# Kernel optimization log

Measured on AMD Instinct MI355X. Metric: run time of the kernel, lower is better.

Reference implementation:

```python
import jax, jax.numpy as jnp
import numpy as np
from jax import lax

BETA = 0.8
THRESHOLD = 1.0
SURROGATE_ALPHA = 4.0  # slope of sigmoid surrogate gradient
EPS = 1e-12            # matches torch F.normalize eps

@jax.custom_vjp
def surrogate_spike(m):
    # forward: hard threshold at THRESHOLD
    return (m >= THRESHOLD).astype(m.dtype)

def _spike_fwd(m):
    return surrogate_spike(m), m

def _spike_bwd(m, g):
    # sigmoid-derivative surrogate gradient around threshold
    s = jax.nn.sigmoid(SURROGATE_ALPHA * (m - THRESHOLD))
    return (g * SURROGATE_ALPHA * s * (1.0 - s),)

surrogate_spike.defvjp(_spike_fwd, _spike_bwd)

def _l2_normalize(x):
    n = jnp.sqrt(jnp.sum(x * x, axis=-1, keepdims=True))
    return x / jnp.maximum(n, EPS)

def setup_inputs() -> dict:
    key = jax.random.key(0)
    k1, k2, k3 = jax.random.split(key, 3)
    B, T, D, F = 4, 2048, 1024, 4096
    mlp_input = jax.random.normal(k1, (B, T, D), dtype=jnp.float32)
    mlp_activation = jax.random.normal(k2, (B, T, F), dtype=jnp.float32)
    W_proj = jax.random.normal(k3, (F, D), dtype=jnp.float32) * (1.0 / np.sqrt(D))
    theta = jnp.ones((F,), dtype=jnp.float32) * THRESHOLD
    return {"mlp_input": mlp_input, "mlp_activation": mlp_activation,
            "W_proj": W_proj, "theta": theta}

def reference(mlp_input, mlp_activation, W_proj, theta):
    B, T, D = mlp_input.shape
    Fdim = W_proj.shape[0]
    # gate_input: (B, T, d_ff) = mlp_input @ W^T
    gate_input = jnp.einsum('btd,fd->btf', mlp_input, W_proj)

    def step(mem, g_t):
        mem = BETA * mem + g_t               # leaky integrate
        spk = surrogate_spike(mem)           # fire
        mem = mem - theta * spk              # soft reset
        return mem, spk

    mem0 = jnp.zeros((B, Fdim), dtype=gate_input.dtype)
    # scan over time: (T, B, d_ff)
    _, spikes = lax.scan(step, mem0, jnp.swapaxes(gate_input, 0, 1))
    lif_gate = jnp.swapaxes(spikes, 0, 1)    # (B, T, d_ff)

    norm_mlp = _l2_normalize(mlp_activation)
    norm_lif = _l2_normalize(lif_gate)
    # cosine similarity of two (already) unit vectors == dot product
    cos = jnp.sum(norm_mlp * norm_lif, axis=-1)
    return 1.0 - jnp.mean(cos)
```

## Files before the change

### kernel.cpp

```cpp
#include <hip/hip_runtime.h>
#include <hip/hip_bf16.h>

typedef unsigned short u16;
typedef unsigned char  u8;
typedef unsigned int   u32;
typedef unsigned long long u64;
typedef __attribute__((ext_vector_type(4)))  int i32x4;
typedef __attribute__((ext_vector_type(16))) int i32x16;

#define T_LEN    2048
#define NB       4
#define K_DIM    1024
#define F_DIM    4096
#define M_FULL   (NB * T_LEN)
#define BETA_C   0.8f
#define THRESH_C 1.0f
#define S8DEC    (6.0f / 127.0f)
#define A_ENC    (127.0f / 6.0f)
#define W_ENC    (127.0f / 0.1875f)
#define C_QUANT  (0.1875f / 127.0f)

__device__ static inline u32 q8pack(float4 v, float s) {
    int q0 = (int)rintf(fminf(fmaxf(v.x * s, -127.f), 127.f));
    int q1 = (int)rintf(fminf(fmaxf(v.y * s, -127.f), 127.f));
    int q2 = (int)rintf(fminf(fmaxf(v.z * s, -127.f), 127.f));
    int q3 = (int)rintf(fminf(fmaxf(v.w * s, -127.f), 127.f));
    return (u32)(q0 & 255) | ((u32)(q1 & 255) << 8) | ((u32)(q2 & 255) << 16) |
           ((u32)(q3 & 255) << 24);
}

__global__ __launch_bounds__(256) void cvt8_kernel(const float* __restrict__ a,
                                                   const float* __restrict__ w,
                                                   u8* __restrict__ oa,
                                                   u8* __restrict__ ow,
                                                   int n4a, int n4tot) {
    int stride = gridDim.x * blockDim.x;
    for (int i = blockIdx.x * blockDim.x + threadIdx.x; i < n4tot; i += stride) {
        bool isA = (i < n4a);
        int j = isA ? i : (i - n4a);
        float4 v = isA ? ((const float4*)a)[j] : ((const float4*)w)[j];
        u32 p = q8pack(v, isA ? A_ENC : W_ENC);
        if (isA) ((u32*)oa)[j] = p; else ((u32*)ow)[j] = p;
    }
}

__device__ static inline void gload_lds16(const void* g, void* l) {
    __builtin_amdgcn_global_load_lds(
        (const __attribute__((address_space(1))) unsigned int*)g,
        (__attribute__((address_space(3))) unsigned int*)l, 16, 0, 0);
}

#define NT 16

__global__ __launch_bounds__(256, 3) void gemm_i8(const u8* __restrict__ A8,
                                                  const u8* __restrict__ W8,
                                                  u8* __restrict__ gateT) {
    __shared__ __attribute__((aligned(16))) char lbytes[32768];

    const int tid  = threadIdx.x;
    const int lane = tid & 63;
    const int w    = tid >> 6;
    const int wm   = w >> 1;
    const int wn   = w & 1;

    int orig = blockIdx.x;
    int wg   = (orig & 7) * 256 + (orig >> 3);
    const int bm = (wg >> 5) * 128;
    const int bn = (wg & 31) * 128;

    const u8* aG  = A8 + (size_t)(bm + (tid & 127)) * K_DIM + (tid >> 7) * 16;
    const u8* wGp = W8 + (size_t)(bn + (tid & 127)) * K_DIM + (tid >> 7) * 16;

#define SG_A(dst, kt) { gload_lds16(aG + (kt),       (dst) + tid * 16);          \
                        gload_lds16(aG + (kt) + 32,  (dst) + 4096 + tid * 16); }
#define SG_B(dst, kt) { gload_lds16(wGp + (kt),      (dst) + 8192 + tid * 16);   \
                        gload_lds16(wGp + (kt) + 32, (dst) + 12288 + tid * 16); }

    i32x16 acc[2][2] = {};

    SG_A(lbytes, 0); SG_B(lbytes, 0);
    __syncthreads();

    for (int t = 0; t < NT; ++t) {
        const int cur = t & 1;
        const char* base = lbytes + cur * 16384;
        char* dN = lbytes + (cur ^ 1) * 16384;

        i32x4 a[2][2], b[2][2];
        const int kgo = (lane >> 5) * 2048;
        const int ar  = (wm * 64 + (lane & 31)) * 16;
        const int br  = (wn * 64 + (lane & 31)) * 16;
#pragma unroll
        for (int ks = 0; ks < 2; ++ks) {
#pragma unroll
            for (int mf = 0; mf < 2; ++mf)
                a[mf][ks] = *(const i32x4*)(base + ks * 4096 + kgo + ar + mf * 512);
#pragma unroll
            for (int nf = 0; nf < 2; ++nf)
                b[nf][ks] = *(const i32x4*)(base + 8192 + ks * 4096 + kgo + br + nf * 512);
        }

        if (t + 1 < NT) { SG_A(dN, (t + 1) * 64); SG_B(dN, (t + 1) * 64); }

#pragma unroll
        for (int mf = 0; mf < 2; ++mf)
#pragma unroll
            for (int nf = 0; nf < 2; ++nf)
#pragma unroll
                for (int ks = 0; ks < 2; ++ks)
                    acc[mf][nf] = __builtin_amdgcn_mfma_i32_32x32x32_i8(
                        a[mf][ks], b[nf][ks], acc[mf][nf], 0, 0, 0);

        __syncthreads();
    }

    u32* clw = (u32*)lbytes;
    const int hl = lane >> 5;
    const int cl = lane & 31;
#pragma unroll
    for (int mf = 0; mf < 2; ++mf)
#pragma unroll
        for (int nf = 0; nf < 2; ++nf) {
            int col = wn * 64 + nf * 32 + cl;
            int r4b = wm * 16 + mf * 8 + hl;
            i32x16 v = acc[mf][nf];
#pragma unroll
            for (int g = 0; g < 4; ++g) {
                int q0 = (int)rintf(fminf(fmaxf((float)v[4*g+0] * C_QUANT, -127.f), 127.f));
                int q1 = (int)rintf(fminf(fmaxf((float)v[4*g+1] * C_QUANT, -127.f), 127.f));
                int q2 = (int)rintf(fminf(fmaxf((float)v[4*g+2] * C_QUANT, -127.f), 127.f));
                int q3 = (int)rintf(fminf(fmaxf((float)v[4*g+3] * C_QUANT, -127.f), 127.f));
                u32 p = (u32)(q0 & 255) | ((u32)(q1 & 255) << 8) |
                        ((u32)(q2 & 255) << 16) | ((u32)(q3 & 255) << 24);
                int row4 = r4b + 2 * g;
                clw[col * 32 + (row4 ^ (col & 31))] = p;
            }
        }
    __syncthreads();
#pragma unroll
    for (int it = 0; it < 4; ++it) {
        int idx = tid + it * 256;
        int col = idx >> 3;
        int tof = idx & 7;
        u32 x0 = clw[col * 32 + ((tof * 4 + 0) ^ (col & 31))];
        u32 x1 = clw[col * 32 + ((tof * 4 + 1) ^ (col & 31))];
        u32 x2 = clw[col * 32 + ((tof * 4 + 2) ^ (col & 31))];
        u32 x3 = clw[col * 32 + ((tof * 4 + 3) ^ (col & 31))];
        uint4 q; q.x = x0; q.y = x1; q.z = x2; q.w = x3;
        *(uint4*)&gateT[(size_t)(bn + col) * M_FULL + bm + tof * 16] = q;
    }
#undef SG_A
#undef SG_B
}

__device__ static inline void lif_group(uint4 v, float& mem, float th,
                                        int lane, u64* pk, int tb, bool doout) {
    u32 ws[4] = {v.x, v.y, v.z, v.w};
#pragma unroll
    for (int w4 = 0; w4 < 4; ++w4) {
#pragma unroll
        for (int by = 0; by < 4; ++by) {
            int q = (int)((signed char)((ws[w4] >> (by * 8)) & 0xffu));
            mem = BETA_C * mem + (float)q * S8DEC;
            bool sp = (mem >= THRESH_C);
            u64 mk = __ballot(sp);
            if (sp) mem -= th;
            if (doout && lane == 0) pk[(size_t)(tb + w4 * 4 + by) * 64] = mk;
        }
    }
}

__global__ __launch_bounds__(256) void lif_kernel(const u8* __restrict__ gateT,
                                                  const float* __restrict__ theta,
                                                  u64* __restrict__ packed) {
    const int tid  = threadIdx.x;
    const int lane = tid & 63;
    const int wid  = blockIdx.x * 4 + (tid >> 6);
    const int fg   = wid & 63;
    const int s    = (wid >> 6) & 15;
    const int b    = wid >> 10;
    const int f    = fg * 64 + lane;
    const int m0   = b * T_LEN + s * 128;
    const float th = theta[f];
    const u8* gp = gateT + (size_t)f * M_FULL + m0;
    u64* pk = packed + (size_t)m0 * 64 + fg;
    float mem = 0.0f;

    if (s == 0) {
        uint4 v0 = *(const uint4*)(gp +   0), v1 = *(const uint4*)(gp +  16);
        uint4 v2 = *(const uint4*)(gp +  32), v3 = *(const uint4*)(gp +  48);
        uint4 v4 = *(const uint4*)(gp +  64), v5 = *(const uint4*)(gp +  80);
        uint4 v6 = *(const uint4*)(gp +  96), v7 = *(const uint4*)(gp + 112);
        lif_group(v0, mem, th, lane, pk,   0, true);
        lif_group(v1, mem, th, lane, pk,  16, true);
        lif_group(v2, mem, th, lane, pk,  32, true);
        lif_group(v3, mem, th, lane, pk,  48, true);
        lif_group(v4, mem, th, lane, pk,  64, true);
        lif_group(v5, mem, th, lane, pk,  80, true);
        lif_group(v6, mem, th, lane, pk,  96, true);
        lif_group(v7, mem, th, lane, pk, 112, true);
    } else {
        const u8* gw = gp - 64;
        uint4 w0 = *(const uint4*)(gw +   0), w1 = *(const uint4*)(gw +  16);
        uint4 w2 = *(const uint4*)(gw +  32), w3 = *(const uint4*)(gw +  48);
        uint4 v0 = *(const uint4*)(gp +   0), v1 = *(const uint4*)(gp +  16);
        uint4 v2 = *(const uint4*)(gp +  32), v3 = *(const uint4*)(gp +  48);
        uint4 v4 = *(const uint4*)(gp +  64), v5 = *(const uint4*)(gp +  80);
        uint4 v6 = *(const uint4*)(gp +  96), v7 = *(const uint4*)(gp + 112);
        lif_group(w0, mem, th, lane, pk, 0, false);
        lif_group(w1, mem, th, lane, pk, 0, false);
        lif_group(w2, mem, th, lane, pk, 0, false);
        lif_group(w3, mem, th, lane, pk, 0, false);
        lif_group(v0, mem, th, lane, pk,   0, true);
        lif_group(v1, mem, th, lane, pk,  16, true);
        lif_group(v2, mem, th, lane, pk,  32, true);
        lif_group(v3, mem, th, lane, pk,  48, true);
        lif_group(v4, mem, th, lane, pk,  64, true);
        lif_group(v5, mem, th, lane, pk,  80, true);
        lif_group(v6, mem, th, lane, pk,  96, true);
        lif_group(v7, mem, th, lane, pk, 112, true);
    }
}

__global__ __launch_bounds__(256) void row_reduce_kernel(const float* __restrict__ act,
                                                         const u64* __restrict__ packed,
                                                         float* __restrict__ row_cos) {
    int row = blockIdx.x;
    int tid = threadIdx.x;
    const float* a = act + (size_t)row * F_DIM + tid * 16;
    u64 wv = packed[(size_t)row * 64 + (tid >> 2)];
    unsigned bits = (unsigned)((wv >> ((tid & 3) * 16)) & 0xFFFFull);

    float dot = 0.f, a2 = 0.f;
    float cnt = (float)__popc(bits);
#pragma unroll
    for (int q = 0; q < 4; ++q) {
        float4 av = ((const float4*)a)[q];
        dot += ((bits >> (q * 4 + 0)) & 1) ? av.x : 0.f;
        dot += ((bits >> (q * 4 + 1)) & 1) ? av.y : 0.f;
        dot += ((bits >> (q * 4 + 2)) & 1) ? av.z : 0.f;
        dot += ((bits >> (q * 4 + 3)) & 1) ? av.w : 0.f;
        a2  += av.x * av.x + av.y * av.y + av.z * av.z + av.w * av.w;
    }
#pragma unroll
    for (int off = 32; off > 0; off >>= 1) {
        dot += __shfl_down(dot, off);
        a2  += __shfl_down(a2, off);
        cnt += __shfl_down(cnt, off);
    }
    __shared__ float sd[4], sa[4], sc[4];
    int w = tid >> 6, lane = tid & 63;
    if (lane == 0) { sd[w] = dot; sa[w] = a2; sc[w] = cnt; }
    __syncthreads();
    if (tid == 0) {
        float D  = sd[0] + sd[1] + sd[2] + sd[3];
        float A2 = sa[0] + sa[1] + sa[2] + sa[3];
        float Cn = sc[0] + sc[1] + sc[2] + sc[3];
        float na = fmaxf(sqrtf(A2), 1e-12f);
        float ns = fmaxf(sqrtf(Cn), 1e-12f);
        row_cos[row] = D / (na * ns);
    }
}

__global__ __launch_bounds__(256) void final_reduce_kernel(const float* __restrict__ row_cos,
                                                           float* __restrict__ out) {
    int tid = threadIdx.x;
    float sum = 0.f;
    for (int i = tid; i < M_FULL; i += 256) sum += row_cos[i];
#pragma unroll
    for (int off = 32; off > 0; off >>= 1) sum += __shfl_down(sum, off);
    __shared__ float sw[4];
    int w = tid >> 6, lane = tid & 63;
    if (lane == 0) sw[w] = sum;
    __syncthreads();
    if (tid == 0) out[0] = 1.0f - (sw[0] + sw[1] + sw[2] + sw[3]) * (1.0f / (float)M_FULL);
}

extern "C" void kernel_launch(void* const* d_in, const int* in_sizes, int n_in,
                              void* d_out, int out_size, void* d_ws, size_t ws_size,
                              hipStream_t stream) {
    const float* mlp_input = (const float*)d_in[0];
    const float* mlp_act   = (const float*)d_in[1];
    const float* W         = (const float*)d_in[2];
    const float* theta     = (const float*)d_in[3];
    float* out = (float*)d_out;

    char* ws = (char*)d_ws;
    size_t off = 0;
    auto alloc = [&](size_t n) { size_t o = off; off = (off + n + 255) & ~(size_t)255; return o; };

    u8* A8        = (u8*)(ws + alloc((size_t)M_FULL * K_DIM));
    u8* W8        = (u8*)(ws + alloc((size_t)F_DIM * K_DIM));
    u64* packed   = (u64*)(ws + alloc((size_t)M_FULL * 64 * 8));
    float* rowcos = (float*)(ws + alloc((size_t)M_FULL * 4));
    u8* gateT     = (u8*)(ws + alloc((size_t)F_DIM * M_FULL));

    const int n4a = M_FULL * K_DIM / 4;
    const int n4t = n4a + F_DIM * K_DIM / 4;
    cvt8_kernel<<<2048, 256, 0, stream>>>(mlp_input, W, A8, W8, n4a, n4t);

    gemm_i8<<<(M_FULL / 128) * (F_DIM / 128), 256, 0, stream>>>(A8, W8, gateT);

    lif_kernel<<<1024, 256, 0, stream>>>(gateT, theta, packed);

    row_reduce_kernel<<<M_FULL, 256, 0, stream>>>(mlp_act, packed, rowcos);
    final_reduce_kernel<<<1, 256, 0, stream>>>(rowcos, out);
}
```

Baseline: 138.9 us.

## Triple-buffer int8 GEMM LDS loads and remap tiles per XCD

Switches the int8 GEMM from double to triple buffering in LDS, so two K-tiles are prefetched ahead. The full syncthreads is replaced by explicit vmcnt waits plus a raw barrier, which lets one stage's loads stay outstanding across iterations. Block-to-tile mapping also changes so each XCD owns a contiguous range of N columns, aiming for better L2 reuse of weights. LDS use rises to 48KB per block, which may limit the three blocks per CU set by the launch bounds. The hand-written waitcnt sequencing risks races if the compiler reorders memory operations.

```diff
diff --git a/kernel.cpp b/kernel.cpp
--- a/kernel.cpp
+++ b/kernel.cpp
@@ -55,7 +55,7 @@
 __global__ __launch_bounds__(256, 3) void gemm_i8(const u8* __restrict__ A8,
                                                   const u8* __restrict__ W8,
                                                   u8* __restrict__ gateT) {
-    __shared__ __attribute__((aligned(16))) char lbytes[32768];
+    __shared__ __attribute__((aligned(16))) char lbytes[49152];
 
     const int tid  = threadIdx.x;
     const int lane = tid & 63;
@@ -64,27 +64,28 @@
     const int wn   = w & 1;
 
     int orig = blockIdx.x;
-    int wg   = (orig & 7) * 256 + (orig >> 3);
-    const int bm = (wg >> 5) * 128;
-    const int bn = (wg & 31) * 128;
+    int xcd  = orig & 7;
+    int loc  = orig >> 3;
+    const int bn = (xcd * 4 + (loc >> 6)) * 128;
+    const int bm = (loc & 63) * 128;
 
     const u8* aG  = A8 + (size_t)(bm + (tid & 127)) * K_DIM + (tid >> 7) * 16;
     const u8* wGp = W8 + (size_t)(bn + (tid & 127)) * K_DIM + (tid >> 7) * 16;
 
-#define SG_A(dst, kt) { gload_lds16(aG + (kt),       (dst) + tid * 16);          \
-                        gload_lds16(aG + (kt) + 32,  (dst) + 4096 + tid * 16); }
-#define SG_B(dst, kt) { gload_lds16(wGp + (kt),      (dst) + 8192 + tid * 16);   \
-                        gload_lds16(wGp + (kt) + 32, (dst) + 12288 + tid * 16); }
+#define SG_T(dst, kt) { gload_lds16(aG + (kt),        (dst) + tid * 16);          \
+                        gload_lds16(aG + (kt) + 32,   (dst) + 4096 + tid * 16);   \
+                        gload_lds16(wGp + (kt),       (dst) + 8192 + tid * 16);   \
+                        gload_lds16(wGp + (kt) + 32,  (dst) + 12288 + tid * 16); }
 
     i32x16 acc[2][2] = {};
 
-    SG_A(lbytes, 0); SG_B(lbytes, 0);
+    SG_T(lbytes, 0);
+    SG_T(lbytes + 16384, 64);
+    asm volatile("s_waitcnt vmcnt(4)" ::: "memory");
     __syncthreads();
 
     for (int t = 0; t < NT; ++t) {
-        const int cur = t & 1;
-        const char* base = lbytes + cur * 16384;
-        char* dN = lbytes + (cur ^ 1) * 16384;
+        const char* base = lbytes + (t % 3) * 16384;
 
         i32x4 a[2][2], b[2][2];
         const int kgo = (lane >> 5) * 2048;
@@ -100,7 +101,7 @@
                 b[nf][ks] = *(const i32x4*)(base + 8192 + ks * 4096 + kgo + br + nf * 512);
         }
 
-        if (t + 1 < NT) { SG_A(dN, (t + 1) * 64); SG_B(dN, (t + 1) * 64); }
+        if (t + 2 < NT) { char* dP = lbytes + ((t + 2) % 3) * 16384; SG_T(dP, (t + 2) * 64); }
 
 #pragma unroll
         for (int mf = 0; mf < 2; ++mf)
@@ -111,7 +112,11 @@
                     acc[mf][nf] = __builtin_amdgcn_mfma_i32_32x32x32_i8(
                         a[mf][ks], b[nf][ks], acc[mf][nf], 0, 0, 0);
 
-        __syncthreads();
+        if (t + 1 < NT) {
+            if (t + 2 < NT) { asm volatile("s_waitcnt vmcnt(4)" ::: "memory"); }
+            else            { asm volatile("s_waitcnt vmcnt(0)" ::: "memory"); }
+        }
+        __builtin_amdgcn_s_barrier();
     }
 
     u32* clw = (u32*)lbytes;
@@ -149,8 +154,7 @@
         uint4 q; q.x = x0; q.y = x1; q.z = x2; q.w = x3;
         *(uint4*)&gateT[(size_t)(bn + col) * M_FULL + bm + tof * 16] = q;
     }
-#undef SG_A
-#undef SG_B
+#undef SG_T
 }
 
 __device__ static inline void lif_group(uint4 v, float& mem, float th,
```

After: 144.0 us. 1.04x slower.
